# Kernel tuning notes

Measured on AMD Instinct MI355X. Metric: run time of the kernel, lower is better.

## Reference

```python
import jax, jax.numpy as jnp
import numpy as np

B, S, HID = 2, 2048, 1024
NH, HD = 16, 64  # op_heads, head_size; op_size = NH*HD = 1024


def setup_inputs() -> dict:
    key = jax.random.key(0)
    k1, k2, k3 = jax.random.split(key, 3)
    hidden_states = jax.random.normal(k1, (B, S, HID), dtype=jnp.float32)
    # Linear weights stored as [in, out] for x @ W + b
    Wqk = jax.random.normal(k2, (HID, 2 * NH * HD), dtype=jnp.float32) * (HID ** -0.5)
    bqk = jnp.zeros((2 * NH * HD,), dtype=jnp.float32)
    Wv = jax.random.normal(k3, (HID, NH * HD), dtype=jnp.float32) * (HID ** -0.5)
    bv = jnp.zeros((NH * HD,), dtype=jnp.float32)
    return {"hidden_states": hidden_states, "Wqk": Wqk, "bqk": bqk, "Wv": Wv, "bv": bv}


def _split_heads(t):
    # [B, S, NH*HD] -> [B, NH, S, HD]
    b, s, _ = t.shape
    return t.reshape(b, s, NH, HD).transpose(0, 2, 1, 3)


def reference(hidden_states, Wqk, bqk, Wv, bv):
    op_size = NH * HD
    qk = hidden_states @ Wqk + bqk                      # [B, S, 2*op_size]
    query, key = qk[..., :op_size], qk[..., op_size:]
    value = hidden_states @ Wv + bv                     # [B, S, op_size]
    q = _split_heads(query)                             # [B, H, S, D]
    k = _split_heads(key)
    v = _split_heads(value)
    # scores: [B, H, Sq, Sk], scaled by sqrt(head_dim) (scale_attn_weights=True)
    scores = jnp.einsum('bhqd,bhkd->bhqk', q, k) / jnp.asarray(HD ** 0.5, q.dtype)
    s = scores.shape[-1]
    causal = jnp.tril(jnp.ones((s, s), dtype=bool))     # [S, S]
    mask_value = jnp.finfo(scores.dtype).min
    scores = jnp.where(causal, scores, mask_value)
    attn = jax.nn.softmax(scores, axis=-1)              # dropout is identity (eval)
    out = jnp.einsum('bhqk,bhkd->bhqd', attn, v)        # [B, H, S, D]
    out = out.transpose(0, 2, 1, 3).reshape(out.shape[0], out.shape[2], NH * HD)
    return out
```

## Files before the change

kernel.cpp:

```cpp
#include <hip/hip_runtime.h>

typedef float floatx4 __attribute__((ext_vector_type(4)));
typedef __bf16 bf16x8 __attribute__((ext_vector_type(8)));
typedef unsigned short u16x8 __attribute__((ext_vector_type(8)));
typedef unsigned short u16x4 __attribute__((ext_vector_type(4)));

#define GLDS16(g, l) __builtin_amdgcn_global_load_lds( \
    (__attribute__((address_space(1))) void*)(g), \
    (__attribute__((address_space(3))) void*)(l), 16, 0, 0)

__device__ __forceinline__ unsigned short f2bf(float f) {
    unsigned u = __float_as_uint(f);
    u += 0x7fffu + ((u >> 16) & 1u);
    return (unsigned short)(u >> 16);
}

__global__ __launch_bounds__(256) void k_convert(const float* __restrict__ in,
                                                 unsigned short* __restrict__ out) {
    int idx = (blockIdx.x * 256 + threadIdx.x) * 8;
    const float4* p = (const float4*)(in + idx);
    float4 f0 = p[0], f1 = p[1];
    u16x8 o;
    o[0] = f2bf(f0.x); o[1] = f2bf(f0.y); o[2] = f2bf(f0.z); o[3] = f2bf(f0.w);
    o[4] = f2bf(f1.x); o[5] = f2bf(f1.y); o[6] = f2bf(f1.z); o[7] = f2bf(f1.w);
    *(u16x8*)(out + idx) = o;
}

__global__ __launch_bounds__(256) void k_transpose(const float* __restrict__ Wqk,
                                                   const float* __restrict__ Wv,
                                                   unsigned short* __restrict__ Wt) {
    __shared__ unsigned short t[64][68];
    const int tid = threadIdx.x;
    const int n0 = blockIdx.x * 64;
    const int k0 = blockIdx.y * 64;
    const int nl = tid & 63;
    const int kb = tid >> 6;
    const int ng = n0 + nl;
#pragma unroll
    for (int i = 0; i < 16; ++i) {
        int kl = kb + i * 4;
        float v = (n0 < 2048) ? Wqk[(size_t)(k0 + kl) * 2048 + ng]
                              : Wv[(size_t)(k0 + kl) * 1024 + (ng - 2048)];
        t[nl][kl] = f2bf(v);
    }
    __syncthreads();
    const int k4 = (tid & 15) * 4;
    const int nb = tid >> 4;
#pragma unroll
    for (int i = 0; i < 4; ++i) {
        int n2 = nb + i * 16;
        u16x4 o;
        o[0] = t[n2][k4]; o[1] = t[n2][k4 + 1]; o[2] = t[n2][k4 + 2]; o[3] = t[n2][k4 + 3];
        *(u16x4*)(Wt + (size_t)(n0 + n2) * 1024 + k0 + k4) = o;
    }
}

__global__ __launch_bounds__(256, 2) void k_gemm_qkv(
    const unsigned short* __restrict__ A,
    const unsigned short* __restrict__ Bt,
    const float* __restrict__ bqk, const float* __restrict__ bvv,
    unsigned short* __restrict__ Qo, unsigned short* __restrict__ Ko,
    unsigned short* __restrict__ VoT) {
    __shared__ unsigned short As[128 * 32];
    __shared__ unsigned short Bs[128 * 32];
    const int tid = threadIdx.x;
    const int lane = tid & 63;
    const int w = tid >> 6;
    const int l15 = lane & 15;
    const int quad = lane >> 4;
    const int m0 = blockIdx.x * 128;
    const int n0 = blockIdx.y * 128;
    const int wm = (w & 1) * 64;
    const int wn = (w >> 1) * 64;
    const int rC = lane >> 2;
    const int kC = (lane & 3) * 8;
    const int c0 = w * 2;

    floatx4 acc[4][4] = {};

    const unsigned short* agp0 = A + (size_t)(m0 + c0 * 16 + rC) * 1024 + kC;
    const unsigned short* agp1 = agp0 + 16 * 1024;
    const unsigned short* bgp0 = Bt + (size_t)(n0 + c0 * 16 + rC) * 1024 + kC;
    const unsigned short* bgp1 = bgp0 + 16 * 1024;
    unsigned short* al = As + c0 * 512;
    unsigned short* bl = Bs + c0 * 512;

    for (int k0 = 0; k0 < 1024; k0 += 32) {
        GLDS16(agp0 + k0, al);
        GLDS16(agp1 + k0, al + 512);
        GLDS16(bgp0 + k0, bl);
        GLDS16(bgp1 + k0, bl + 512);
        __syncthreads();
        const unsigned short* ap = As + (wm + l15) * 32 + quad * 8;
        const unsigned short* bp = Bs + (wn + l15) * 32 + quad * 8;
        bf16x8 af[4], bfr[4];
#pragma unroll
        for (int mi = 0; mi < 4; ++mi) af[mi] = *(const bf16x8*)(ap + mi * 16 * 32);
#pragma unroll
        for (int ni = 0; ni < 4; ++ni) bfr[ni] = *(const bf16x8*)(bp + ni * 16 * 32);
#pragma unroll
        for (int mi = 0; mi < 4; ++mi)
#pragma unroll
            for (int ni = 0; ni < 4; ++ni)
                acc[mi][ni] = __builtin_amdgcn_mfma_f32_16x16x32_bf16(af[mi], bfr[ni],
                                                                      acc[mi][ni], 0, 0, 0);
        __syncthreads();
    }
#pragma unroll
    for (int ni = 0; ni < 4; ++ni) {
        const int n = n0 + wn + ni * 16 + l15;
        if (n < 2048) {
            const float bias = bqk[n];
            const bool isQ = n < 1024;
            unsigned short* dst = isQ ? Qo : Ko;
            const int hd = isQ ? n : n - 1024;
            const float scale = isQ ? 0.125f : 1.0f;
            const int h = hd >> 6, d = hd & 63;
#pragma unroll
            for (int mi = 0; mi < 4; ++mi)
#pragma unroll
                for (int r = 0; r < 4; ++r) {
                    const int m = m0 + wm + mi * 16 + (quad << 2) + r;
                    const int b = m >> 11, s = m & 2047;
                    dst[((size_t)(b * 16 + h) * 2048 + s) * 64 + d] =
                        f2bf((acc[mi][ni][r] + bias) * scale);
                }
        } else {
            const float bias = bvv[n - 2048];
            const int hd = n - 2048;
            const int h = hd >> 6, d = hd & 63;
#pragma unroll
            for (int mi = 0; mi < 4; ++mi) {
                const int m = m0 + wm + mi * 16 + (quad << 2);
                const int b = m >> 11, s = m & 2047;
                u16x4 o4;
#pragma unroll
                for (int r = 0; r < 4; ++r) o4[r] = f2bf(acc[mi][ni][r] + bias);
                *(u16x4*)(VoT + ((size_t)(b * 16 + h) * 64 + d) * 2048 + s) = o4;
            }
        }
    }
}

__global__ __launch_bounds__(256, 2) void k_attn(
    const unsigned short* __restrict__ Q, const unsigned short* __restrict__ K,
    const unsigned short* __restrict__ Vt, float* __restrict__ out) {
    __shared__ unsigned short Ks[64 * 72];
    __shared__ unsigned short Vs[64 * 72];
    __shared__ unsigned short Ps[4][16 * 72];
    const int tid = threadIdx.x;
    const int lane = tid & 63;
    const int w = tid >> 6;
    const int l15 = lane & 15;
    const int quad = lane >> 4;
    const int bh = blockIdx.x >> 4;
    const int p = blockIdx.x & 15;
    const size_t base = (size_t)bh * (2048 * 64);

    const int r8 = lane >> 3;
    const int c8 = (lane & 7) * 8;
    unsigned short* kls0 = &Ks[(w * 16 + r8) * 72 + c8];
    unsigned short* kls1 = &Ks[(w * 16 + 8 + r8) * 72 + c8];
    unsigned short* vls0 = &Vs[(w * 16 + r8) * 72 + c8];
    unsigned short* vls1 = &Vs[(w * 16 + 8 + r8) * 72 + c8];
    const unsigned short* kg = K + base + (size_t)(w * 16 + r8) * 64 + c8;
    const unsigned short* vg = Vt + base + (size_t)(w * 16 + r8) * 2048 + c8;

    const int b = bh >> 4, h = bh & 15;

    for (int pass = 0; pass < 2; ++pass) {
        const int qt = pass ? (31 - p) : p;
        const int qw = qt * 64 + w * 16;

        bf16x8 aQ[2];
        {
            const unsigned short* qp = Q + base + (size_t)(qw + l15) * 64 + quad * 8;
            aQ[0] = *(const bf16x8*)qp;
            aQ[1] = *(const bf16x8*)(qp + 32);
        }
        floatx4 o[4] = {};
        float mrow[4] = {-3e38f, -3e38f, -3e38f, -3e38f};
        float lrow[4] = {0.f, 0.f, 0.f, 0.f};

        u16x8 kr0 = *(const u16x8*)(kg);
        u16x8 kr1 = *(const u16x8*)(kg + 512);
        u16x8 vr0 = *(const u16x8*)(vg);
        u16x8 vr1 = *(const u16x8*)(vg + 8 * 2048);

        for (int t = 0; t <= qt; ++t) {
            __syncthreads();
            *(u16x8*)kls0 = kr0; *(u16x8*)kls1 = kr1;
            *(u16x8*)vls0 = vr0; *(u16x8*)vls1 = vr1;
            __syncthreads();
            if (t < qt) {
                const int kv1 = (t + 1) * 64;
                kr0 = *(const u16x8*)(kg + (size_t)kv1 * 64);
                kr1 = *(const u16x8*)(kg + (size_t)kv1 * 64 + 512);
                vr0 = *(const u16x8*)(vg + kv1);
                vr1 = *(const u16x8*)(vg + kv1 + 8 * 2048);
            }

            floatx4 st[4] = {};
#pragma unroll
            for (int kk = 0; kk < 2; ++kk)
#pragma unroll
                for (int nt = 0; nt < 4; ++nt) {
                    bf16x8 bk = *(const bf16x8*)&Ks[(nt * 16 + l15) * 72 + kk * 32 + quad * 8];
                    st[nt] = __builtin_amdgcn_mfma_f32_16x16x32_bf16(aQ[kk], bk, st[nt], 0, 0, 0);
                }

            if (t == qt) {
                const int kvb = t * 64 + l15;
                const int qg0 = qw + (quad << 2);
#pragma unroll
                for (int nt = 0; nt < 4; ++nt)
#pragma unroll
                    for (int r = 0; r < 4; ++r)
                        if (kvb + nt * 16 > qg0 + r) st[nt][r] = -3e38f;
            }

            float mcur[4] = {-3e38f, -3e38f, -3e38f, -3e38f};
#pragma unroll
            for (int nt = 0; nt < 4; ++nt)
#pragma unroll
                for (int r = 0; r < 4; ++r) mcur[r] = fmaxf(mcur[r], st[nt][r]);
#pragma unroll
            for (int off = 1; off < 16; off <<= 1)
#pragma unroll
                for (int r = 0; r < 4; ++r) mcur[r] = fmaxf(mcur[r], __shfl_xor(mcur[r], off, 64));
            float alpha[4], lsum[4];
#pragma unroll
            for (int r = 0; r < 4; ++r) {
                float mnew = fmaxf(mrow[r], mcur[r]);
                alpha[r] = __expf(mrow[r] - mnew);
                mrow[r] = mnew;
                lsum[r] = 0.f;
            }
#pragma unroll
            for (int nt = 0; nt < 4; ++nt)
#pragma unroll
                for (int r = 0; r < 4; ++r) {
                    float pv = __expf(st[nt][r] - mrow[r]);
                    st[nt][r] = pv;
                    lsum[r] += pv;
                }
            unsigned short* pw = &Ps[w][0];
#pragma unroll
            for (int nt = 0; nt < 4; ++nt)
#pragma unroll
                for (int r = 0; r < 4; ++r)
                    pw[((quad << 2) + r) * 72 + nt * 16 + l15] = f2bf(st[nt][r]);
#pragma unroll
            for (int off = 1; off < 16; off <<= 1)
#pragma unroll
                for (int r = 0; r < 4; ++r) lsum[r] += __shfl_xor(lsum[r], off, 64);
#pragma unroll
            for (int r = 0; r < 4; ++r) lrow[r] = lrow[r] * alpha[r] + lsum[r];
#pragma unroll
            for (int dt = 0; dt < 4; ++dt)
#pragma unroll
                for (int r = 0; r < 4; ++r) o[dt][r] *= alpha[r];
#pragma unroll
            for (int kk = 0; kk < 2; ++kk) {
                bf16x8 apf = *(const bf16x8*)&pw[l15 * 72 + kk * 32 + quad * 8];
#pragma unroll
                for (int dt = 0; dt < 4; ++dt) {
                    bf16x8 bvf = *(const bf16x8*)&Vs[(dt * 16 + l15) * 72 + kk * 32 + quad * 8];
                    o[dt] = __builtin_amdgcn_mfma_f32_16x16x32_bf16(apf, bvf, o[dt], 0, 0, 0);
                }
            }
        }
#pragma unroll
        for (int r = 0; r < 4; ++r) {
            const int qg = qw + (quad << 2) + r;
            const float inv = 1.0f / lrow[r];
            float* op = out + (size_t)(b * 2048 + qg) * 1024 + h * 64 + l15;
#pragma unroll
            for (int dt = 0; dt < 4; ++dt) op[dt * 16] = o[dt][r] * inv;
        }
    }
}

extern "C" void kernel_launch(void* const* d_in, const int* in_sizes, int n_in,
                              void* d_out, int out_size, void* d_ws, size_t ws_size,
                              hipStream_t stream) {
    const float* hidden = (const float*)d_in[0];
    const float* Wqk    = (const float*)d_in[1];
    const float* bqk    = (const float*)d_in[2];
    const float* Wv     = (const float*)d_in[3];
    const float* bvv    = (const float*)d_in[4];
    float* out = (float*)d_out;

    unsigned short* Abf = (unsigned short*)d_ws;
    unsigned short* Wt  = Abf + 4096 * 1024;
    unsigned short* Qo  = Wt + 3072 * 1024;
    unsigned short* Ko  = Qo + 32 * 2048 * 64;
    unsigned short* VoT = Ko + 32 * 2048 * 64;

    k_convert<<<2048, 256, 0, stream>>>(hidden, Abf);
    k_transpose<<<dim3(48, 16), 256, 0, stream>>>(Wqk, Wv, Wt);
    k_gemm_qkv<<<dim3(32, 24), 256, 0, stream>>>(Abf, Wt, bqk, bvv, Qo, Ko, VoT);
    k_attn<<<512, 256, 0, stream>>>(Qo, Ko, VoT, out);
}
```

Baseline: 184.3 us.

## Rewrite attention with 32x32 MFMA, register-resident P, and direct LDS loads

Rewrites the attention kernel to use 32x32x16 bf16 MFMA with each lane owning one query row. The S tile is computed transposed (K as A operand), so P stays in registers and is repacked through cross-half shuffles instead of being round-tripped through LDS. The row max and sum reductions shrink to a single shuffle. K and V are loaded with global_load_lds into a swizzle-free fragment layout. Blocks become 128 threads, one 64-query tile each, launched longest-first over 1024 blocks instead of paired passes, and the register prefetch double-buffer is dropped, so load latency is no longer hidden behind compute.

```diff
diff --git a/kernel.cpp b/kernel.cpp
--- a/kernel.cpp
+++ b/kernel.cpp
@@ -1,6 +1,7 @@
 #include <hip/hip_runtime.h>
 
 typedef float floatx4 __attribute__((ext_vector_type(4)));
+typedef float floatx16 __attribute__((ext_vector_type(16)));
 typedef __bf16 bf16x8 __attribute__((ext_vector_type(8)));
 typedef unsigned short u16x8 __attribute__((ext_vector_type(8)));
 typedef unsigned short u16x4 __attribute__((ext_vector_type(4)));
@@ -14,6 +15,19 @@
     u += 0x7fffu + ((u >> 16) & 1u);
     return (unsigned short)(u >> 16);
 }
+
+#if __has_builtin(__builtin_amdgcn_cvt_pk_bf16_f32)
+__device__ __forceinline__ unsigned pk2(float a, float b) {
+    typedef __bf16 bf16x2 __attribute__((ext_vector_type(2)));
+    union { bf16x2 v; unsigned u; } cv;
+    cv.v = __builtin_amdgcn_cvt_pk_bf16_f32(a, b);
+    return cv.u;
+}
+#else
+__device__ __forceinline__ unsigned pk2(float a, float b) {
+    return (unsigned)f2bf(a) | ((unsigned)f2bf(b) << 16);
+}
+#endif
 
 __global__ __launch_bounds__(256) void k_convert(const float* __restrict__ in,
                                                  unsigned short* __restrict__ out) {
@@ -142,143 +156,125 @@
     }
 }
 
-__global__ __launch_bounds__(256, 2) void k_attn(
+__global__ __launch_bounds__(128, 4) void k_attn(
     const unsigned short* __restrict__ Q, const unsigned short* __restrict__ K,
     const unsigned short* __restrict__ Vt, float* __restrict__ out) {
-    __shared__ unsigned short Ks[64 * 72];
-    __shared__ unsigned short Vs[64 * 72];
-    __shared__ unsigned short Ps[4][16 * 72];
+    __shared__ __align__(16) unsigned short Ks[8 * 512];
+    __shared__ __align__(16) unsigned short Vs[8 * 512];
     const int tid = threadIdx.x;
     const int lane = tid & 63;
     const int w = tid >> 6;
-    const int l15 = lane & 15;
-    const int quad = lane >> 4;
-    const int bh = blockIdx.x >> 4;
-    const int p = blockIdx.x & 15;
+    const int c = lane & 31;
+    const int hh = lane >> 5;
+    const int gb = blockIdx.x;
+    const int u = 31 - (gb >> 5);
+    const int bh = ((gb & 7) << 2) | ((gb >> 3) & 3);
     const size_t base = (size_t)bh * (2048 * 64);
 
-    const int r8 = lane >> 3;
-    const int c8 = (lane & 7) * 8;
-    unsigned short* kls0 = &Ks[(w * 16 + r8) * 72 + c8];
-    unsigned short* kls1 = &Ks[(w * 16 + 8 + r8) * 72 + c8];
-    unsigned short* vls0 = &Vs[(w * 16 + r8) * 72 + c8];
-    unsigned short* vls1 = &Vs[(w * 16 + 8 + r8) * 72 + c8];
-    const unsigned short* kg = K + base + (size_t)(w * 16 + r8) * 64 + c8;
-    const unsigned short* vg = Vt + base + (size_t)(w * 16 + r8) * 2048 + c8;
-
-    const int b = bh >> 4, h = bh & 15;
-
-    for (int pass = 0; pass < 2; ++pass) {
-        const int qt = pass ? (31 - p) : p;
-        const int qw = qt * 64 + w * 16;
-
-        bf16x8 aQ[2];
-        {
-            const unsigned short* qp = Q + base + (size_t)(qw + l15) * 64 + quad * 8;
-            aQ[0] = *(const bf16x8*)qp;
-            aQ[1] = *(const bf16x8*)(qp + 32);
+    const int q_rel = w * 32 + c;
+    const int q_abs = u * 64 + q_rel;
+
+    bf16x8 qf[4];
+    {
+        const unsigned short* qp = Q + base + (size_t)q_abs * 64 + hh * 8;
+#pragma unroll
+        for (int kb = 0; kb < 4; ++kb) qf[kb] = *(const bf16x8*)(qp + kb * 16);
+    }
+
+    const unsigned short* kgp = K + base + (size_t)(w * 32 + c) * 64 + hh * 8;
+    const unsigned short* vgp = Vt + base + (size_t)(w * 32 + c) * 2048 + hh * 8;
+    unsigned short* kls = Ks + (w * 4) * 512;
+    unsigned short* vls = Vs + (w * 4) * 512;
+
+    floatx16 zero = {};
+    floatx16 o2[2] = {};
+    float mrow = -3e38f, lrow = 0.f;
+
+    for (int t = 0; t <= u; ++t) {
+        __syncthreads();
+#pragma unroll
+        for (int kb = 0; kb < 4; ++kb)
+            GLDS16(kgp + t * 4096 + kb * 16, kls + kb * 512);
+#pragma unroll
+        for (int m = 0; m < 4; ++m)
+            GLDS16(vgp + t * 64 + m * 16, vls + m * 512);
+        __syncthreads();
+
+        floatx16 st[2]; st[0] = zero; st[1] = zero;
+#pragma unroll
+        for (int gg = 0; gg < 2; ++gg)
+#pragma unroll
+            for (int kb = 0; kb < 4; ++kb) {
+                bf16x8 kf = *(const bf16x8*)&Ks[(gg * 4 + kb) * 512 + lane * 8];
+                st[gg] = __builtin_amdgcn_mfma_f32_32x32x16_bf16(kf, qf[kb], st[gg], 0, 0, 0);
+            }
+
+        if (t == u) {
+#pragma unroll
+            for (int gg = 0; gg < 2; ++gg)
+#pragma unroll
+                for (int i = 0; i < 16; ++i) {
+                    int kv_rel = gg * 32 + (i & 3) + 8 * (i >> 2) + 4 * hh;
+                    if (kv_rel > q_rel) st[gg][i] = -3e38f;
+                }
         }
-        floatx4 o[4] = {};
-        float mrow[4] = {-3e38f, -3e38f, -3e38f, -3e38f};
-        float lrow[4] = {0.f, 0.f, 0.f, 0.f};
-
-        u16x8 kr0 = *(const u16x8*)(kg);
-        u16x8 kr1 = *(const u16x8*)(kg + 512);
-        u16x8 vr0 = *(const u16x8*)(vg);
-        u16x8 vr1 = *(const u16x8*)(vg + 8 * 2048);
-
-        for (int t = 0; t <= qt; ++t) {
-            __syncthreads();
-            *(u16x8*)kls0 = kr0; *(u16x8*)kls1 = kr1;
-            *(u16x8*)vls0 = vr0; *(u16x8*)vls1 = vr1;
-            __syncthreads();
-            if (t < qt) {
-                const int kv1 = (t + 1) * 64;
-                kr0 = *(const u16x8*)(kg + (size_t)kv1 * 64);
-                kr1 = *(const u16x8*)(kg + (size_t)kv1 * 64 + 512);
-                vr0 = *(const u16x8*)(vg + kv1);
-                vr1 = *(const u16x8*)(vg + kv1 + 8 * 2048);
+
+        float mc = -3e38f;
+#pragma unroll
+        for (int gg = 0; gg < 2; ++gg)
+#pragma unroll
+            for (int i = 0; i < 16; ++i) mc = fmaxf(mc, st[gg][i]);
+        mc = fmaxf(mc, __shfl_xor(mc, 32, 64));
+        const float mnew = fmaxf(mrow, mc);
+        const float alpha = __expf(mrow - mnew);
+        mrow = mnew;
+        float ls = 0.f;
+#pragma unroll
+        for (int gg = 0; gg < 2; ++gg)
+#pragma unroll
+            for (int i = 0; i < 16; ++i) {
+                float p = __expf(st[gg][i] - mnew);
+                st[gg][i] = p;
+                ls += p;
             }
-
-            floatx4 st[4] = {};
-#pragma unroll
-            for (int kk = 0; kk < 2; ++kk)
-#pragma unroll
-                for (int nt = 0; nt < 4; ++nt) {
-                    bf16x8 bk = *(const bf16x8*)&Ks[(nt * 16 + l15) * 72 + kk * 32 + quad * 8];
-                    st[nt] = __builtin_amdgcn_mfma_f32_16x16x32_bf16(aQ[kk], bk, st[nt], 0, 0, 0);
-                }
-
-            if (t == qt) {
-                const int kvb = t * 64 + l15;
-                const int qg0 = qw + (quad << 2);
-#pragma unroll
-                for (int nt = 0; nt < 4; ++nt)
-#pragma unroll
-                    for (int r = 0; r < 4; ++r)
-                        if (kvb + nt * 16 > qg0 + r) st[nt][r] = -3e38f;
-            }
-
-            float mcur[4] = {-3e38f, -3e38f, -3e38f, -3e38f};
-#pragma unroll
-            for (int nt = 0; nt < 4; ++nt)
-#pragma unroll
-                for (int r = 0; r < 4; ++r) mcur[r] = fmaxf(mcur[r], st[nt][r]);
-#pragma unroll
-            for (int off = 1; off < 16; off <<= 1)
-#pragma unroll
-                for (int r = 0; r < 4; ++r) mcur[r] = fmaxf(mcur[r], __shfl_xor(mcur[r], off, 64));
-            float alpha[4], lsum[4];
-#pragma unroll
-            for (int r = 0; r < 4; ++r) {
-                float mnew = fmaxf(mrow[r], mcur[r]);
-                alpha[r] = __expf(mrow[r] - mnew);
-                mrow[r] = mnew;
-                lsum[r] = 0.f;
-            }
-#pragma unroll
-            for (int nt = 0; nt < 4; ++nt)
-#pragma unroll
-                for (int r = 0; r < 4; ++r) {
-                    float pv = __expf(st[nt][r] - mrow[r]);
-                    st[nt][r] = pv;
-                    lsum[r] += pv;
-                }
-            unsigned short* pw = &Ps[w][0];
-#pragma unroll
-            for (int nt = 0; nt < 4; ++nt)
-#pragma unroll
-                for (int r = 0; r < 4; ++r)
-                    pw[((quad << 2) + r) * 72 + nt * 16 + l15] = f2bf(st[nt][r]);
-#pragma unroll
-            for (int off = 1; off < 16; off <<= 1)
-#pragma unroll
-                for (int r = 0; r < 4; ++r) lsum[r] += __shfl_xor(lsum[r], off, 64);
-#pragma unroll
-            for (int r = 0; r < 4; ++r) lrow[r] = lrow[r] * alpha[r] + lsum[r];
-#pragma unroll
-            for (int dt = 0; dt < 4; ++dt)
-#pragma unroll
-                for (int r = 0; r < 4; ++r) o[dt][r] *= alpha[r];
-#pragma unroll
-            for (int kk = 0; kk < 2; ++kk) {
-                bf16x8 apf = *(const bf16x8*)&pw[l15 * 72 + kk * 32 + quad * 8];
-#pragma unroll
-                for (int dt = 0; dt < 4; ++dt) {
-                    bf16x8 bvf = *(const bf16x8*)&Vs[(dt * 16 + l15) * 72 + kk * 32 + quad * 8];
-                    o[dt] = __builtin_amdgcn_mfma_f32_16x16x32_bf16(apf, bvf, o[dt], 0, 0, 0);
-                }
+        ls += __shfl_xor(ls, 32, 64);
+        lrow = lrow * alpha + ls;
+#pragma unroll
+        for (int dt = 0; dt < 2; ++dt) o2[dt] *= alpha;
+
+#pragma unroll
+        for (int mb = 0; mb < 4; ++mb) {
+            const int gg = mb >> 1, rb = (mb & 1) * 8;
+            unsigned p0 = pk2(st[gg][rb + 0], st[gg][rb + 1]);
+            unsigned p1 = pk2(st[gg][rb + 2], st[gg][rb + 3]);
+            unsigned p2 = pk2(st[gg][rb + 4], st[gg][rb + 5]);
+            unsigned p3 = pk2(st[gg][rb + 6], st[gg][rb + 7]);
+            unsigned sA = hh ? p0 : p2;
+            unsigned sB = hh ? p1 : p3;
+            unsigned rA = (unsigned)__shfl_xor((int)sA, 32, 64);
+            unsigned rB = (unsigned)__shfl_xor((int)sB, 32, 64);
+            union { unsigned u4[4]; bf16x8 v; } pf;
+            if (hh == 0) { pf.u4[0] = p0; pf.u4[1] = p1; pf.u4[2] = rA; pf.u4[3] = rB; }
+            else         { pf.u4[0] = rA; pf.u4[1] = rB; pf.u4[2] = p2; pf.u4[3] = p3; }
+#pragma unroll
+            for (int dt = 0; dt < 2; ++dt) {
+                bf16x8 vf = *(const bf16x8*)&Vs[(dt * 4 + mb) * 512 + lane * 8];
+                o2[dt] = __builtin_amdgcn_mfma_f32_32x32x16_bf16(vf, pf.v, o2[dt], 0, 0, 0);
             }
         }
-#pragma unroll
-        for (int r = 0; r < 4; ++r) {
-            const int qg = qw + (quad << 2) + r;
-            const float inv = 1.0f / lrow[r];
-            float* op = out + (size_t)(b * 2048 + qg) * 1024 + h * 64 + l15;
-#pragma unroll
-            for (int dt = 0; dt < 4; ++dt) op[dt * 16] = o[dt][r] * inv;
+    }
+
+    const int b = bh >> 4, head = bh & 15;
+    const float inv = 1.0f / lrow;
+    float* op = out + (size_t)(b * 2048 + q_abs) * 1024 + head * 64;
+#pragma unroll
+    for (int dt = 0; dt < 2; ++dt)
+#pragma unroll
+        for (int rr = 0; rr < 4; ++rr) {
+            float4 v4 = make_float4(o2[dt][rr * 4 + 0] * inv, o2[dt][rr * 4 + 1] * inv,
+                                    o2[dt][rr * 4 + 2] * inv, o2[dt][rr * 4 + 3] * inv);
+            *(float4*)(op + dt * 32 + rr * 8 + hh * 4) = v4;
         }
-    }
 }
 
 extern "C" void kernel_launch(void* const* d_in, const int* in_sizes, int n_in,
@@ -300,5 +296,5 @@
     k_convert<<<2048, 256, 0, stream>>>(hidden, Abf);
     k_transpose<<<dim3(48, 16), 256, 0, stream>>>(Wqk, Wv, Wt);
     k_gemm_qkv<<<dim3(32, 24), 256, 0, stream>>>(Abf, Wt, bqk, bvv, Qo, Ko, VoT);
-    k_attn<<<512, 256, 0, stream>>>(Qo, Ko, VoT, out);
-}
+    k_attn<<<1024, 128, 0, stream>>>(Qo, Ko, VoT, out);
+}
```

Measured after the change: 177.6 us. 3.6% less time.
